# Optimization experiments

Hardware: AMD Instinct MI355X
Metric: run time of the kernel (lower is better)

The kernel has to match this reference:

```python
import jax, jax.numpy as jnp
import numpy as np
import math

D_MODEL = 768
NUM_HEADS = 12
HEAD_SIZE = D_MODEL // NUM_HEADS
BATCH = 4
SEQ = 2048


def setup_inputs() -> dict:
    key = jax.random.key(0)
    ks = jax.random.split(key, 11)
    s = 1.0 / math.sqrt(D_MODEL)
    inp = {
        "queries": jax.random.normal(ks[0], (BATCH, SEQ, D_MODEL), jnp.float32),
        "keys": jax.random.normal(ks[1], (BATCH, SEQ, D_MODEL), jnp.float32),
        "values": jax.random.normal(ks[2], (BATCH, SEQ, D_MODEL), jnp.float32),
        # nn.Linear weights are (out_features, in_features); y = x @ W.T + b
        "W_Q": jax.random.uniform(ks[3], (D_MODEL, D_MODEL), jnp.float32, -s, s),
        "b_Q": jax.random.uniform(ks[4], (D_MODEL,), jnp.float32, -s, s),
        "W_K": jax.random.uniform(ks[5], (D_MODEL, D_MODEL), jnp.float32, -s, s),
        "b_K": jax.random.uniform(ks[6], (D_MODEL,), jnp.float32, -s, s),
        "W_V": jax.random.uniform(ks[7], (D_MODEL, D_MODEL), jnp.float32, -s, s),
        "b_V": jax.random.uniform(ks[8], (D_MODEL,), jnp.float32, -s, s),
        "W_O": jax.random.uniform(ks[9], (D_MODEL, D_MODEL), jnp.float32, -s, s),
        "b_O": jax.random.uniform(ks[10], (D_MODEL,), jnp.float32, -s, s),
    }
    return inp


def _split_heads(x):
    # [B, S, H*d] -> [B, H, S, d]
    B, S, _ = x.shape
    return x.reshape(B, S, NUM_HEADS, HEAD_SIZE).transpose(0, 2, 1, 3)


def _merge_heads(x):
    # [B, H, S, d] -> [B, S, H*d]
    B, H, S, d = x.shape
    return x.transpose(0, 2, 1, 3).reshape(B, S, H * d)


def reference(queries, keys, values, W_Q, b_Q, W_K, b_K, W_V, b_V, W_O, b_O):
    Q = _split_heads(queries @ W_Q.T + b_Q)  # [B,H,S,d]
    K = _split_heads(keys @ W_K.T + b_K)
    V = _split_heads(values @ W_V.T + b_V)

    scale = 1.0 / math.sqrt(HEAD_SIZE)
    scores = jnp.einsum("bhqd,bhkd->bhqk", Q, K) * scale  # [B,H,S,S]
    causal = jnp.tril(jnp.ones((SEQ, SEQ), dtype=bool))  # [S,S]
    scores = jnp.where(causal, scores, -jnp.inf)
    attn = jax.nn.softmax(scores, axis=-1)  # causal weights, zeros above diag
    attended = jnp.einsum("bhqk,bhkd->bhqd", attn, V)
    context = _merge_heads(attended)  # [B,S,D]
    outputs = context @ W_O.T + b_O
    return outputs
```

## Files before the change

kernel.cpp:

```cpp
#include <hip/hip_runtime.h>
#include <hip/hip_bf16.h>

#define DM 768
#define NH 12
#define HD 64
#define B_ 4
#define S_ 2048
#define MT (B_*S_)

typedef unsigned short u16;
typedef __attribute__((ext_vector_type(8))) short bf16x8;
typedef __attribute__((ext_vector_type(4))) float f32x4;
typedef __attribute__((ext_vector_type(4))) short s16x4;

__device__ __forceinline__ u16 f2bf(float f) {
    union { float f; unsigned u; } x; x.f = f;
    unsigned r = x.u + 0x7fffu + ((x.u >> 16) & 1u);
    return (u16)(r >> 16);
}

__device__ __forceinline__ unsigned pk2(float a, float b) {
    union { __hip_bfloat162 h; unsigned u; } cv;
    cv.h = __float22bfloat162_rn(float2{a, b});
    return cv.u;
}

#define GLD_LDS(gp, lp) \
    __builtin_amdgcn_global_load_lds( \
        (const __attribute__((address_space(1))) void*)(gp), \
        (__attribute__((address_space(3))) void*)(lp), 16, 0, 0)

__global__ void cvt3_kernel(const float* __restrict__ s0, const float* __restrict__ s1,
                            const float* __restrict__ s2,
                            u16* __restrict__ d0, u16* __restrict__ d1, u16* __restrict__ d2,
                            int blocksPer) {
    int sel = blockIdx.x / blocksPer;
    int rel = blockIdx.x % blocksPer;
    const float* s = (sel == 0) ? s0 : (sel == 1) ? s1 : s2;
    u16* d = (sel == 0) ? d0 : (sel == 1) ? d1 : d2;
    int i = (rel * 256 + threadIdx.x) * 4;
    float4 v = *(const float4*)(s + i);
    s16x4 o;
    o.x = (short)f2bf(v.x); o.y = (short)f2bf(v.y);
    o.z = (short)f2bf(v.z); o.w = (short)f2bf(v.w);
    *(s16x4*)(d + i) = o;
}

__global__ void cvt4_kernel(const float* __restrict__ s0, const float* __restrict__ s1,
                            const float* __restrict__ s2, const float* __restrict__ s3,
                            u16* __restrict__ d0, u16* __restrict__ d1,
                            u16* __restrict__ d2, u16* __restrict__ d3,
                            int blocksPer) {
    int sel = blockIdx.x / blocksPer;
    int rel = blockIdx.x % blocksPer;
    const float* s = (sel == 0) ? s0 : (sel == 1) ? s1 : (sel == 2) ? s2 : s3;
    u16* d = (sel == 0) ? d0 : (sel == 1) ? d1 : (sel == 2) ? d2 : d3;
    int i = (rel * 256 + threadIdx.x) * 4;
    float4 v = *(const float4*)(s + i);
    s16x4 o;
    o.x = (short)f2bf(v.x); o.y = (short)f2bf(v.y);
    o.z = (short)f2bf(v.z); o.w = (short)f2bf(v.w);
    *(s16x4*)(d + i) = o;
}

__device__ __forceinline__ void gemm_core_128(
    const u16* __restrict__ A, const u16* __restrict__ B,
    int m0, int n0, u16* As, u16* Bs, f32x4 acc[4][4])
{
    const int tid = threadIdx.x;
    const int lane = tid & 63;
    const int lr = lane & 15, quad = lane >> 4;
    const int wave = tid >> 6;
    const int wm = (wave & 1) * 64, wn = (wave >> 1) * 64;

    for (int ks = 0; ks < 24; ++ks) {
        #pragma unroll
        for (int r = 0; r < 2; ++r) {
            int idx = r * 256 + tid;
            int row = idx >> 2, col = (idx & 3) * 8;
            GLD_LDS(A + (size_t)(m0 + row) * DM + ks * 32 + col, As + idx * 8);
            GLD_LDS(B + (size_t)(n0 + row) * DM + ks * 32 + col, Bs + idx * 8);
        }
        __syncthreads();
        bf16x8 a[4], b[4];
        #pragma unroll
        for (int i = 0; i < 4; ++i) a[i] = *(const bf16x8*)(As + (wm + i * 16 + lr) * 32 + quad * 8);
        #pragma unroll
        for (int j = 0; j < 4; ++j) b[j] = *(const bf16x8*)(Bs + (wn + j * 16 + lr) * 32 + quad * 8);
        #pragma unroll
        for (int i = 0; i < 4; ++i)
            #pragma unroll
            for (int j = 0; j < 4; ++j)
                acc[i][j] = __builtin_amdgcn_mfma_f32_16x16x32_bf16(a[i], b[j], acc[i][j], 0, 0, 0);
        __syncthreads();
    }
}

__global__ __launch_bounds__(256) void qkv_gemm(
    const u16* __restrict__ Xq, const u16* __restrict__ Xk, const u16* __restrict__ Xv,
    const u16* __restrict__ Wq, const u16* __restrict__ Wk, const u16* __restrict__ Wv,
    const float* __restrict__ bQ, const float* __restrict__ bK, const float* __restrict__ bV,
    u16* __restrict__ Qo, u16* __restrict__ Ko, u16* __restrict__ VTo)
{
    __shared__ __align__(16) u16 As[128 * 32];
    __shared__ __align__(16) u16 Bs[128 * 32];

    const int mat = blockIdx.x / 384;
    const int t   = blockIdx.x % 384;
    const int mt  = t / 6, nt = t % 6;
    const u16* X = (mat == 0) ? Xq : (mat == 1 ? Xk : Xv);
    const u16* W = (mat == 0) ? Wq : (mat == 1 ? Wk : Wv);
    const float* bias = (mat == 0) ? bQ : (mat == 1 ? bK : bV);

    const int lane = threadIdx.x & 63;
    const int lr = lane & 15, quad = lane >> 4;
    const int wave = threadIdx.x >> 6;
    const int m0 = mt * 128 + (wave & 1) * 64;
    const int n0 = nt * 128 + (wave >> 1) * 64;

    f32x4 acc[4][4] = {};
    gemm_core_128(X, W, mt * 128, nt * 128, As, Bs, acc);

    const int bb = m0 / S_, s0 = m0 % S_, h = n0 / HD;
    if (mat < 2) {
        u16* O = (mat == 0) ? Qo : Ko;
        const float qs = (mat == 0) ? 0.18033688011112042f : 1.0f;
        #pragma unroll
        for (int jj = 0; jj < 4; ++jj) {
            float bv = bias[n0 + jj * 16 + lr];
            #pragma unroll
            for (int i = 0; i < 4; ++i)
                #pragma unroll
                for (int r = 0; r < 4; ++r) {
                    int s = s0 + i * 16 + quad * 4 + r;
                    O[((size_t)(bb * NH + h) * S_ + s) * HD + jj * 16 + lr] = f2bf((acc[i][jj][r] + bv) * qs);
                }
        }
    } else {
        #pragma unroll
        for (int jj = 0; jj < 4; ++jj) {
            float bv = bias[n0 + jj * 16 + lr];
            #pragma unroll
            for (int i = 0; i < 4; ++i) {
                int s = s0 + i * 16 + quad * 4;
                s16x4 o;
                o.x = (short)f2bf(acc[i][jj][0] + bv);
                o.y = (short)f2bf(acc[i][jj][1] + bv);
                o.z = (short)f2bf(acc[i][jj][2] + bv);
                o.w = (short)f2bf(acc[i][jj][3] + bv);
                *(s16x4*)(VTo + ((size_t)(bb * NH + h) * HD + jj * 16 + lr) * S_ + s) = o;
            }
        }
    }
}

__global__ __launch_bounds__(64, 3) void attn_kernel(
    const u16* __restrict__ Q, const u16* __restrict__ K,
    const u16* __restrict__ VT, u16* __restrict__ CTX)
{
    const int lane = threadIdx.x;
    const int lr = lane & 15, quad = lane >> 4;
    const int xcd = blockIdx.x & 7;
    const int idx = blockIdx.x >> 3;
    const int bh  = xcd * 6 + (idx % 6);
    const int qw  = 63 - (idx / 6);
    const int q0  = qw * 32;
    const u16* Qb = Q  + (size_t)bh * S_ * HD;
    const u16* Kb = K  + (size_t)bh * S_ * HD;
    const u16* Vb = VT + (size_t)bh * HD * S_;

    __shared__ __align__(16) float pbuf[2][16][68];

    bf16x8 aq[2][2];
    #pragma unroll
    for (int mi = 0; mi < 2; ++mi)
        #pragma unroll
        for (int kk = 0; kk < 2; ++kk)
            aq[mi][kk] = *(const bf16x8*)(Qb + (size_t)(q0 + mi * 16 + lr) * HD + kk * 32 + quad * 8);

    f32x4 o[2][4] = {};
    f32x4 lacc[2] = {};
    bf16x8 ones;
    #pragma unroll
    for (int j = 0; j < 8; ++j) ones[j] = (short)0x3F80;

    const int ktmax = (q0 + 31) >> 6;

    bf16x8 bk[4][2];
    #pragma unroll
    for (int nt = 0; nt < 4; ++nt)
        #pragma unroll
        for (int kk = 0; kk < 2; ++kk)
            bk[nt][kk] = *(const bf16x8*)(Kb + (size_t)(nt * 16 + lr) * HD + kk * 32 + quad * 8);

    for (int kt = 0; kt <= ktmax; ++kt) {
        const int k0 = kt << 6;

        bf16x8 bv[4][2];
        #pragma unroll
        for (int nv = 0; nv < 4; ++nv)
            #pragma unroll
            for (int c = 0; c < 2; ++c)
                bv[nv][c] = *(const bf16x8*)(Vb + (size_t)(nv * 16 + lr) * S_ + k0 + c * 32 + quad * 8);

        f32x4 sc[2][4];
        #pragma unroll
        for (int mi = 0; mi < 2; ++mi)
            #pragma unroll
            for (int nt = 0; nt < 4; ++nt) {
                f32x4 z = {0.f, 0.f, 0.f, 0.f};
                z = __builtin_amdgcn_mfma_f32_16x16x32_bf16(aq[mi][0], bk[nt][0], z, 0, 0, 0);
                z = __builtin_amdgcn_mfma_f32_16x16x32_bf16(aq[mi][1], bk[nt][1], z, 0, 0, 0);
                sc[mi][nt] = z;
            }

        if (kt < ktmax) {
            #pragma unroll
            for (int nt = 0; nt < 4; ++nt)
                #pragma unroll
                for (int kk = 0; kk < 2; ++kk)
                    bk[nt][kk] = *(const bf16x8*)(Kb + (size_t)(k0 + 64 + nt * 16 + lr) * HD + kk * 32 + quad * 8);
        }

        if (kt == ktmax) {
            #pragma unroll
            for (int mi = 0; mi < 2; ++mi)
                #pragma unroll
                for (int nt = 0; nt < 4; ++nt)
                    #pragma unroll
                    for (int r = 0; r < 4; ++r) {
                        int row = q0 + mi * 16 + quad * 4 + r;
                        int col = k0 + nt * 16 + lr;
                        if (col > row) sc[mi][nt][r] = -INFINITY;
                    }
        }

        #pragma unroll
        for (int mi = 0; mi < 2; ++mi)
            #pragma unroll
            for (int nt = 0; nt < 4; ++nt)
                #pragma unroll
                for (int r = 0; r < 4; ++r)
                    sc[mi][nt][r] = exp2f(sc[mi][nt][r]);

        #pragma unroll
        for (int mi = 0; mi < 2; ++mi)
            #pragma unroll
            for (int r = 0; r < 4; ++r) {
                float* bp = &pbuf[mi][quad * 4 + r][lr];
                bp[0]  = sc[mi][0][r];
                bp[16] = sc[mi][1][r];
                bp[32] = sc[mi][2][r];
                bp[48] = sc[mi][3][r];
            }

        bf16x8 pa[2][2];
        #pragma unroll
        for (int mi = 0; mi < 2; ++mi)
            #pragma unroll
            for (int c = 0; c < 2; ++c) {
                const float* rp = &pbuf[mi][lr][c * 32 + quad * 8];
                union { unsigned u[4]; bf16x8 v; } P;
                #pragma unroll
                for (int p = 0; p < 4; ++p)
                    P.u[p] = pk2(rp[2 * p], rp[2 * p + 1]);
                pa[mi][c] = P.v;
            }

        #pragma unroll
        for (int mi = 0; mi < 2; ++mi) {
            lacc[mi] = __builtin_amdgcn_mfma_f32_16x16x32_bf16(pa[mi][0], ones, lacc[mi], 0, 0, 0);
            lacc[mi] = __builtin_amdgcn_mfma_f32_16x16x32_bf16(pa[mi][1], ones, lacc[mi], 0, 0, 0);
            #pragma unroll
            for (int nv = 0; nv < 4; ++nv) {
                o[mi][nv] = __builtin_amdgcn_mfma_f32_16x16x32_bf16(pa[mi][0], bv[nv][0], o[mi][nv], 0, 0, 0);
                o[mi][nv] = __builtin_amdgcn_mfma_f32_16x16x32_bf16(pa[mi][1], bv[nv][1], o[mi][nv], 0, 0, 0);
            }
        }
    }

    const int bb = bh / NH, h = bh % NH;
    #pragma unroll
    for (int mi = 0; mi < 2; ++mi) {
        f32x4 inv;
        #pragma unroll
        for (int r = 0; r < 4; ++r) inv[r] = 1.0f / lacc[mi][r];
        #pragma unroll
        for (int nv = 0; nv < 4; ++nv)
            #pragma unroll
            for (int r = 0; r < 4; ++r)
                CTX[(size_t)(bb * S_ + q0 + mi * 16 + quad * 4 + r) * DM + h * HD + nv * 16 + lr]
                    = f2bf(o[mi][nv][r] * inv[r]);
    }
}

__global__ __launch_bounds__(256) void o_gemm(
    const u16* __restrict__ X, const u16* __restrict__ W,
    const float* __restrict__ bias, float* __restrict__ Out)
{
    __shared__ __align__(16) u16 As[128 * 32];
    __shared__ __align__(16) u16 Bs[128 * 32];

    const int mt = blockIdx.x / 6, nt = blockIdx.x % 6;
    const int lane = threadIdx.x & 63;
    const int lr = lane & 15, quad = lane >> 4;
    const int wave = threadIdx.x >> 6;
    const int m0 = mt * 128 + (wave & 1) * 64;
    const int n0 = nt * 128 + (wave >> 1) * 64;

    f32x4 acc[4][4] = {};
    gemm_core_128(X, W, mt * 128, nt * 128, As, Bs, acc);

    #pragma unroll
    for (int jj = 0; jj < 4; ++jj) {
        float bv = bias[n0 + jj * 16 + lr];
        #pragma unroll
        for (int i = 0; i < 4; ++i)
            #pragma unroll
            for (int r = 0; r < 4; ++r)
                Out[(size_t)(m0 + i * 16 + quad * 4 + r) * DM + n0 + jj * 16 + lr] = acc[i][jj][r] + bv;
    }
}

extern "C" void kernel_launch(void* const* d_in, const int* in_sizes, int n_in,
                              void* d_out, int out_size, void* d_ws, size_t ws_size,
                              hipStream_t stream) {
    const float* q  = (const float*)d_in[0];
    const float* k  = (const float*)d_in[1];
    const float* v  = (const float*)d_in[2];
    const float* WQ = (const float*)d_in[3];
    const float* bQ = (const float*)d_in[4];
    const float* WK = (const float*)d_in[5];
    const float* bK = (const float*)d_in[6];
    const float* WV = (const float*)d_in[7];
    const float* bV = (const float*)d_in[8];
    const float* WO = (const float*)d_in[9];
    const float* bO = (const float*)d_in[10];

    char* ws = (char*)d_ws;
    const size_t SZ_X = (size_t)MT * DM * 2;
    const size_t SZ_W = (size_t)DM * DM * 2;
    u16* Xq = (u16*)(ws);
    u16* Xk = (u16*)(ws + SZ_X);
    u16* Xv = (u16*)(ws + 2 * SZ_X);
    u16* Wq = (u16*)(ws + 3 * SZ_X);
    u16* Wk = (u16*)(ws + 3 * SZ_X + SZ_W);
    u16* Wv = (u16*)(ws + 3 * SZ_X + 2 * SZ_W);
    u16* Wo = (u16*)(ws + 3 * SZ_X + 3 * SZ_W);
    u16* Qh  = (u16*)(ws + 3 * SZ_X + 4 * SZ_W);
    u16* Kh  = (u16*)(ws + 4 * SZ_X + 4 * SZ_W);
    u16* VTh = (u16*)(ws + 5 * SZ_X + 4 * SZ_W);
    u16* CTX = Xq;

    const int nX = MT * DM;
    const int nW = DM * DM;
    cvt3_kernel<<<3 * (nX / 1024), 256, 0, stream>>>(q, k, v, Xq, Xk, Xv, nX / 1024);
    cvt4_kernel<<<4 * (nW / 1024), 256, 0, stream>>>(WQ, WK, WV, WO, Wq, Wk, Wv, Wo, nW / 1024);

    qkv_gemm<<<1152, 256, 0, stream>>>(Xq, Xk, Xv, Wq, Wk, Wv, bQ, bK, bV, Qh, Kh, VTh);
    attn_kernel<<<3072, 64, 0, stream>>>(Qh, Kh, VTh, CTX);
    o_gemm<<<384, 256, 0, stream>>>(CTX, Wo, bO, (float*)d_out);
}
```

Measured before the change: 322.7 us.

## Split attention key loop across four waves with shared-memory reduction

Each attention block now has four waves instead of one. The waves interleave over key tiles (kt = wave, wave+4, ...), and their partial output and row-sum accumulators are combined through shared memory in a two-step tree reduction before wave 0 writes the context. The goal is more parallelism per query tile, which shortens the long serial causal loops for late query blocks. In exchange it drops the K-tile register prefetch, adds syncthreads and reduction traffic, and lets each wave process a load-imbalanced subset of tiles.

```diff
diff --git a/kernel.cpp b/kernel.cpp
--- a/kernel.cpp
+++ b/kernel.cpp
@@ -154,11 +154,13 @@
     }
 }
 
-__global__ __launch_bounds__(64, 3) void attn_kernel(
+__global__ __launch_bounds__(256, 5) void attn_kernel(
     const u16* __restrict__ Q, const u16* __restrict__ K,
     const u16* __restrict__ VT, u16* __restrict__ CTX)
 {
-    const int lane = threadIdx.x;
+    const int tid = threadIdx.x;
+    const int wave = tid >> 6;
+    const int lane = tid & 63;
     const int lr = lane & 15, quad = lane >> 4;
     const int xcd = blockIdx.x & 7;
     const int idx = blockIdx.x >> 3;
@@ -169,7 +171,8 @@
     const u16* Kb = K  + (size_t)bh * S_ * HD;
     const u16* Vb = VT + (size_t)bh * HD * S_;
 
-    __shared__ __align__(16) float pbuf[2][16][68];
+    __shared__ __align__(16) float smem[2 * 64 * 44];
+    float* pbuf = smem + wave * (16 * 68);
 
     bf16x8 aq[2][2];
     #pragma unroll
@@ -186,16 +189,15 @@
 
     const int ktmax = (q0 + 31) >> 6;
 
-    bf16x8 bk[4][2];
-    #pragma unroll
-    for (int nt = 0; nt < 4; ++nt)
-        #pragma unroll
-        for (int kk = 0; kk < 2; ++kk)
-            bk[nt][kk] = *(const bf16x8*)(Kb + (size_t)(nt * 16 + lr) * HD + kk * 32 + quad * 8);
-
-    for (int kt = 0; kt <= ktmax; ++kt) {
+    for (int kt = wave; kt <= ktmax; kt += 4) {
         const int k0 = kt << 6;
 
+        bf16x8 bk[4][2];
+        #pragma unroll
+        for (int nt = 0; nt < 4; ++nt)
+            #pragma unroll
+            for (int kk = 0; kk < 2; ++kk)
+                bk[nt][kk] = *(const bf16x8*)(Kb + (size_t)(k0 + nt * 16 + lr) * HD + kk * 32 + quad * 8);
         bf16x8 bv[4][2];
         #pragma unroll
         for (int nv = 0; nv < 4; ++nv)
@@ -213,14 +215,6 @@
                 z = __builtin_amdgcn_mfma_f32_16x16x32_bf16(aq[mi][1], bk[nt][1], z, 0, 0, 0);
                 sc[mi][nt] = z;
             }
-
-        if (kt < ktmax) {
-            #pragma unroll
-            for (int nt = 0; nt < 4; ++nt)
-                #pragma unroll
-                for (int kk = 0; kk < 2; ++kk)
-                    bk[nt][kk] = *(const bf16x8*)(Kb + (size_t)(k0 + 64 + nt * 16 + lr) * HD + kk * 32 + quad * 8);
-        }
 
         if (kt == ktmax) {
             #pragma unroll
@@ -243,29 +237,27 @@
                 for (int r = 0; r < 4; ++r)
                     sc[mi][nt][r] = exp2f(sc[mi][nt][r]);
 
-        #pragma unroll
-        for (int mi = 0; mi < 2; ++mi)
+        bf16x8 pa[2][2];
+        #pragma unroll
+        for (int mi = 0; mi < 2; ++mi) {
             #pragma unroll
             for (int r = 0; r < 4; ++r) {
-                float* bp = &pbuf[mi][quad * 4 + r][lr];
+                float* bp = &pbuf[(quad * 4 + r) * 68 + lr];
                 bp[0]  = sc[mi][0][r];
                 bp[16] = sc[mi][1][r];
                 bp[32] = sc[mi][2][r];
                 bp[48] = sc[mi][3][r];
             }
-
-        bf16x8 pa[2][2];
-        #pragma unroll
-        for (int mi = 0; mi < 2; ++mi)
             #pragma unroll
             for (int c = 0; c < 2; ++c) {
-                const float* rp = &pbuf[mi][lr][c * 32 + quad * 8];
+                const float* rp = &pbuf[lr * 68 + c * 32 + quad * 8];
                 union { unsigned u[4]; bf16x8 v; } P;
                 #pragma unroll
                 for (int p = 0; p < 4; ++p)
                     P.u[p] = pk2(rp[2 * p], rp[2 * p + 1]);
                 pa[mi][c] = P.v;
             }
+        }
 
         #pragma unroll
         for (int mi = 0; mi < 2; ++mi) {
@@ -279,18 +271,63 @@
         }
     }
 
-    const int bb = bh / NH, h = bh % NH;
-    #pragma unroll
-    for (int mi = 0; mi < 2; ++mi) {
-        f32x4 inv;
-        #pragma unroll
-        for (int r = 0; r < 4; ++r) inv[r] = 1.0f / lacc[mi][r];
-        #pragma unroll
-        for (int nv = 0; nv < 4; ++nv)
-            #pragma unroll
-            for (int r = 0; r < 4; ++r)
-                CTX[(size_t)(bb * S_ + q0 + mi * 16 + quad * 4 + r) * DM + h * HD + nv * 16 + lr]
-                    = f2bf(o[mi][nv][r] * inv[r]);
+    __syncthreads();
+    float* red = smem;
+    if (wave >= 2) {
+        float* rp = red + (wave - 2) * (64 * 44) + lane * 44;
+        #pragma unroll
+        for (int mi = 0; mi < 2; ++mi) {
+            #pragma unroll
+            for (int nv = 0; nv < 4; ++nv)
+                *(f32x4*)(rp + (mi * 4 + nv) * 4) = o[mi][nv];
+            *(f32x4*)(rp + 32 + mi * 4) = lacc[mi];
+        }
+    }
+    __syncthreads();
+    if (wave < 2) {
+        const float* rp = red + wave * (64 * 44) + lane * 44;
+        #pragma unroll
+        for (int mi = 0; mi < 2; ++mi) {
+            #pragma unroll
+            for (int nv = 0; nv < 4; ++nv)
+                o[mi][nv] += *(const f32x4*)(rp + (mi * 4 + nv) * 4);
+            lacc[mi] += *(const f32x4*)(rp + 32 + mi * 4);
+        }
+    }
+    __syncthreads();
+    if (wave == 1) {
+        float* rp = red + lane * 44;
+        #pragma unroll
+        for (int mi = 0; mi < 2; ++mi) {
+            #pragma unroll
+            for (int nv = 0; nv < 4; ++nv)
+                *(f32x4*)(rp + (mi * 4 + nv) * 4) = o[mi][nv];
+            *(f32x4*)(rp + 32 + mi * 4) = lacc[mi];
+        }
+    }
+    __syncthreads();
+    if (wave == 0) {
+        const float* rp = red + lane * 44;
+        #pragma unroll
+        for (int mi = 0; mi < 2; ++mi) {
+            #pragma unroll
+            for (int nv = 0; nv < 4; ++nv)
+                o[mi][nv] += *(const f32x4*)(rp + (mi * 4 + nv) * 4);
+            lacc[mi] += *(const f32x4*)(rp + 32 + mi * 4);
+        }
+        const int bb = bh / NH, h = bh % NH;
+        #pragma unroll
+        for (int mi = 0; mi < 2; ++mi) {
+            f32x4 inv;
+            #pragma unroll
+            for (int r = 0; r < 4; ++r) inv[r] = 1.0f / lacc[mi][r];
+            #pragma unroll
+            for (int nv = 0; nv < 4; ++nv)
+                #pragma unroll
+                for (int r = 0; r < 4; ++r)
+                    CTX[(size_t)(bb * S_ + q0 + mi * 16 + quad * 4 + r) * DM + h * HD + nv * 16 + lr]
+                        = f2bf(o[mi][nv][r] * inv[r]);
+        }
     }
 }
 
@@ -358,6 +395,6 @@
     cvt4_kernel<<<4 * (nW / 1024), 256, 0, stream>>>(WQ, WK, WV, WO, Wq, Wk, Wv, Wo, nW / 1024);
 
     qkv_gemm<<<1152, 256, 0, stream>>>(Xq, Xk, Xv, Wq, Wk, Wv, bQ, bK, bV, Qh, Kh, VTh);
-    attn_kernel<<<3072, 64, 0, stream>>>(Qh, Kh, VTh, CTX);
+    attn_kernel<<<3072, 256, 0, stream>>>(Qh, Kh, VTh, CTX);
     o_gemm<<<384, 256, 0, stream>>>(CTX, Wo, bO, (float*)d_out);
 }
```

Result: slower. 449.3 us (+39.3%).
